# Kernel tuning notes

Hardware: AMD Instinct MI355X
Metric: run time of the kernel (lower is better)

## Reference

```python
import jax, jax.numpy as jnp
import numpy as np

N = 100000
E = 1600000
D = 128
L = 2
NEG_SLOPE = 0.2
LN_EPS = 1e-5


def setup_inputs() -> dict:
    key = jax.random.key(0)
    ks = jax.random.split(key, 12)
    x = jax.random.normal(ks[0], (N, D), dtype=jnp.float32)
    src = jax.random.randint(ks[1], (E,), 0, N)
    dst = jax.random.randint(ks[2], (E,), 0, N)
    dst = jnp.where(src == dst, (dst + 1) % N, dst)  # no pre-existing self-loops
    edge_index = jnp.stack([src, dst]).astype(jnp.int64)
    edge_weight = jax.random.uniform(ks[3], (E,), dtype=jnp.float32)
    s = 1.0 / np.sqrt(D)
    W = jax.random.normal(ks[4], (L, D, D), dtype=jnp.float32) * s
    att_src = jax.random.normal(ks[5], (L, D), dtype=jnp.float32) * s
    att_dst = jax.random.normal(ks[6], (L, D), dtype=jnp.float32) * s
    lin_edge_w = jax.random.normal(ks[7], (L, D), dtype=jnp.float32) * s  # Linear(1, D) weight
    att_edge = jax.random.normal(ks[8], (L, D), dtype=jnp.float32) * s
    bias = jnp.zeros((L, D), dtype=jnp.float32)
    ln_gamma = jnp.ones((D,), dtype=jnp.float32)
    ln_beta = jnp.zeros((D,), dtype=jnp.float32)
    return {"x": x, "edge_index": edge_index, "edge_weight": edge_weight,
            "W": W, "att_src": att_src, "att_dst": att_dst,
            "lin_edge_w": lin_edge_w, "att_edge": att_edge, "bias": bias,
            "ln_gamma": ln_gamma, "ln_beta": ln_beta}


def _gat_layer(x, src_f, dst_f, ew_f, W, a_src, a_dst, lew, a_edge, b):
    # x: [N, D]; src_f/dst_f/ew_f already include self-loops -> [E+N]
    h = x @ W                      # [N, D]
    alpha_s = h @ a_src            # [N]
    alpha_d = h @ a_dst            # [N]
    # edge_attr = ew[:,None] * lew; (edge_attr * att_edge).sum(-1) == ew * (lew . att_edge)
    alpha_e = ew_f * jnp.dot(lew, a_edge)           # [E+N]
    logits = jax.nn.leaky_relu(alpha_s[src_f] + alpha_d[dst_f] + alpha_e, NEG_SLOPE)
    # segment softmax over incoming edges of each destination node
    m = jax.ops.segment_max(logits, dst_f, num_segments=N)   # every node has a self-loop
    p = jnp.exp(logits - m[dst_f])
    z = jax.ops.segment_sum(p, dst_f, num_segments=N)
    coef = p / z[dst_f]                                      # [E+N]
    out = jax.ops.segment_sum(h[src_f] * coef[:, None], dst_f, num_segments=N)
    return out + b


def reference(x, edge_index, edge_weight, W, att_src, att_dst, lin_edge_w, att_edge, bias, ln_gamma, ln_beta):
    src, dst = edge_index[0], edge_index[1]
    # add_self_loops with fill_value='mean': loop weight = mean of incoming edge weights
    deg = jax.ops.segment_sum(jnp.ones_like(edge_weight), dst, num_segments=N)
    loop_w = jax.ops.segment_sum(edge_weight, dst, num_segments=N) / jnp.maximum(deg, 1.0)
    ar = jnp.arange(N)
    src_f = jnp.concatenate([src, ar])
    dst_f = jnp.concatenate([dst, ar])
    ew_f = jnp.concatenate([edge_weight, loop_w])
    xx = x
    for l in range(L):
        xx = _gat_layer(xx, src_f, dst_f, ew_f, W[l], att_src[l], att_dst[l],
                        lin_edge_w[l], att_edge[l], bias[l])
        xx = jax.nn.gelu(xx, approximate=False)
    xx = x + xx
    mu = jnp.mean(xx, axis=-1, keepdims=True)
    var = jnp.mean((xx - mu) ** 2, axis=-1, keepdims=True)
    return (xx - mu) * jax.lax.rsqrt(var + LN_EPS) * ln_gamma + ln_beta
```

## Files before the change

### kernel.cpp

```cpp
#include <hip/hip_runtime.h>
#include <hip/hip_bf16.h>
#include <math.h>

#define N_NODES 100000
#define N_EDGES 1600000
#define D 128
#define NEG 0.2f
#define LN_EPS 1e-5f

#define GEMM_BLOCKS ((N_NODES + 63) / 64)
#define PLACE_BLOCKS 1563

typedef __attribute__((ext_vector_type(8))) short bf16x8;
typedef __attribute__((ext_vector_type(4))) float f32x4;

__device__ __forceinline__ float lrelu(float v){ return fmaxf(v, NEG * v); }
__device__ __forceinline__ float gelu_exact(float v){ return 0.5f * v * (1.0f + erff(v * 0.7071067811865476f)); }
__device__ __forceinline__ float wave_sum(float v){
#pragma unroll
  for (int o = 32; o; o >>= 1) v += __shfl_xor(v, o, 64);
  return v;
}
__device__ __forceinline__ unsigned short f2bf(float f){
  __hip_bfloat16 h = __float2bfloat16(f);
  return *(unsigned short*)&h;
}
__device__ __forceinline__ float bf_lo(unsigned u){ return __uint_as_float(u << 16); }
__device__ __forceinline__ float bf_hi(unsigned u){ return __uint_as_float(u & 0xFFFF0000u); }

__global__ __launch_bounds__(256) void k_prep(const float* __restrict__ W,
                                              unsigned short* __restrict__ wfrag,
                                              const float* __restrict__ lew,
                                              const float* __restrict__ ae,
                                              float* __restrict__ c_e){
  if (threadIdx.x < 128){
    int l = threadIdx.x >> 6;
    int lane = threadIdx.x & 63;
    const float* a = lew + l * D;
    const float* b = ae + l * D;
    float v = a[lane] * b[lane] + a[64 + lane] * b[64 + lane];
    v = wave_sum(v);
    if (lane == 0) c_e[l] = v;
  }
#pragma unroll
  for (int it = 0; it < 16; it++){
    int slot = it * 256 + threadIdx.x;
    int lane = slot & 63;
    int kc   = (slot >> 6) & 3;
    int ct   = (slot >> 8) & 7;
    int l    = (slot >> 11) & 1;
    int quad = lane >> 4, n = (lane & 15) + ct * 16;
    const float* Wl = W + l * D * D;
    bf16x8 v;
#pragma unroll
    for (int j = 0; j < 8; j++){
      int k = kc * 32 + quad * 8 + j;
      v[j] = (short)f2bf(Wl[k * D + n]);
    }
    *(bf16x8*)(wfrag + (size_t)slot * 8) = v;
  }
}

__device__ __forceinline__ void gemm_mfma(int gb,
                                          const float* __restrict__ xin,
                                          const unsigned short* __restrict__ wfrag_l,
                                          const float* __restrict__ att_s,
                                          const float* __restrict__ att_d,
                                          unsigned short* __restrict__ hb,
                                          float* __restrict__ alpha_s,
                                          float* __restrict__ alpha_d){
  __shared__ __align__(16) unsigned short hstage[64 * 136];
  int tid = threadIdx.x;
  int wv = tid >> 6, lane = tid & 63;
  int quad = lane >> 4, c15 = lane & 15;
  int row0 = gb * 64 + wv * 16;

  int arow = min(row0 + c15, N_NODES - 1);
  const float* xr = xin + (size_t)arow * D;
  bf16x8 a[4];
#pragma unroll
  for (int kc = 0; kc < 4; kc++){
    float4 p = *(const float4*)(xr + kc * 32 + quad * 8);
    float4 q = *(const float4*)(xr + kc * 32 + quad * 8 + 4);
    bf16x8 t;
    t[0] = (short)f2bf(p.x); t[1] = (short)f2bf(p.y);
    t[2] = (short)f2bf(p.z); t[3] = (short)f2bf(p.w);
    t[4] = (short)f2bf(q.x); t[5] = (short)f2bf(q.y);
    t[6] = (short)f2bf(q.z); t[7] = (short)f2bf(q.w);
    a[kc] = t;
  }

  f32x4 acc[8];
#pragma unroll
  for (int ct = 0; ct < 8; ct++) acc[ct] = (f32x4){0.f, 0.f, 0.f, 0.f};

#pragma unroll
  for (int ct = 0; ct < 8; ct++){
#pragma unroll
    for (int kc = 0; kc < 4; kc++){
      bf16x8 b = *(const bf16x8*)(wfrag_l + ((size_t)(ct * 4 + kc) * 64 + lane) * 8);
      acc[ct] = __builtin_amdgcn_mfma_f32_16x16x32_bf16(a[kc], b, acc[ct], 0, 0, 0);
    }
  }

  float attsv[8], attdv[8];
#pragma unroll
  for (int ct = 0; ct < 8; ct++){
    attsv[ct] = att_s[ct * 16 + c15];
    attdv[ct] = att_d[ct * 16 + c15];
  }
#pragma unroll
  for (int reg = 0; reg < 4; reg++){
    float ps = 0.f, pd = 0.f;
#pragma unroll
    for (int ct = 0; ct < 8; ct++){
      ps += acc[ct][reg] * attsv[ct];
      pd += acc[ct][reg] * attdv[ct];
    }
#pragma unroll
    for (int o = 8; o; o >>= 1){
      ps += __shfl_xor(ps, o, 64);
      pd += __shfl_xor(pd, o, 64);
    }
    int row = row0 + quad * 4 + reg;
    if (c15 == reg && row < N_NODES){ alpha_s[row] = ps; alpha_d[row] = pd; }
  }

#pragma unroll
  for (int ct = 0; ct < 8; ct++)
#pragma unroll
    for (int reg = 0; reg < 4; reg++)
      hstage[(wv * 16 + quad * 4 + reg) * 136 + ct * 16 + c15] = f2bf(acc[ct][reg]);
  __syncthreads();
#pragma unroll
  for (int i = 0; i < 4; i++){
    int flat = i * 256 + tid;
    int row = flat >> 4, c = flat & 15;
    int grow = gb * 64 + row;
    if (grow < N_NODES)
      *(uint4*)(hb + (size_t)grow * D + c * 8) = *(const uint4*)(hstage + row * 136 + c * 8);
  }
}

__global__ __launch_bounds__(256, 4) void k_gemm1_place(const float* __restrict__ xin,
                                                        const unsigned short* __restrict__ wfrag,
                                                        const float* __restrict__ att_s,
                                                        const float* __restrict__ att_d,
                                                        unsigned short* __restrict__ hb,
                                                        float* __restrict__ alpha_s,
                                                        float* __restrict__ alpha_d,
                                                        const int* __restrict__ ei,
                                                        const float* __restrict__ ew,
                                                        int* __restrict__ counter,
                                                        int2* __restrict__ csr, int cap){
  if (blockIdx.x < GEMM_BLOCKS){
    gemm_mfma(blockIdx.x, xin, wfrag, att_s, att_d, hb, alpha_s, alpha_d);
  } else {
    int pb = blockIdx.x - GEMM_BLOCKS;
    int e0 = pb * 1024 + threadIdx.x;
    int ss[4], dd[4], pp[4]; float wwv[4]; bool va[4];
#pragma unroll
    for (int i = 0; i < 4; i++){
      int e = e0 + i * 256;
      va[i] = e < N_EDGES;
      ss[i] = va[i] ? ei[e] : 0;
      dd[i] = va[i] ? ei[N_EDGES + e] : 0;
      wwv[i] = va[i] ? ew[e] : 0.f;
    }
#pragma unroll
    for (int i = 0; i < 4; i++) if (va[i]) pp[i] = atomicAdd(&counter[dd[i]], 1);
#pragma unroll
    for (int i = 0; i < 4; i++)
      if (va[i] && pp[i] < cap)
        csr[(size_t)dd[i] * cap + pp[i]] = make_int2(ss[i], __float_as_int(wwv[i]));
  }
}

__global__ __launch_bounds__(256, 4) void k_gemm_alpha(const float* __restrict__ xin,
                                                       const unsigned short* __restrict__ wfrag,
                                                       const float* __restrict__ att_s,
                                                       const float* __restrict__ att_d,
                                                       unsigned short* __restrict__ hb,
                                                       float* __restrict__ alpha_s,
                                                       float* __restrict__ alpha_d){
  gemm_mfma(blockIdx.x, xin, wfrag, att_s, att_d, hb, alpha_s, alpha_d);
}

template<bool LN>
__global__ __launch_bounds__(256) void k_agg(const unsigned short* __restrict__ hb,
                                             const float* __restrict__ alpha_s,
                                             const float* __restrict__ alpha_d,
                                             const int* __restrict__ counter,
                                             const int2* __restrict__ csr, int cap,
                                             const float* __restrict__ c_e, int layer,
                                             const float* __restrict__ bias,
                                             const float* __restrict__ xres,
                                             const float* __restrict__ gamma,
                                             const float* __restrict__ beta,
                                             float* __restrict__ outp){
  int lane = threadIdx.x & 63;
  int cg = lane & 15;
  int qbase = lane & 48;
  int n = blockIdx.x * 16 + (threadIdx.x >> 4);
  float c = c_e[layer];
  int deg = counter[n];
  int dg = min(deg, cap);
  size_t rs = (size_t)n * cap;
  float ad = alpha_d[n];

  float z = 0.f, wsum = 0.f;
  float acc[8];
#pragma unroll
  for (int k = 0; k < 8; k++) acc[k] = 0.f;

  for (int base = 0; base < dg; base += 16){
    int j = base + cg;
    float p = 0.f; int s = 0;
    if (j < dg){
      int2 eg = csr[rs + j];
      s = eg.x;
      float w = __int_as_float(eg.y);
      wsum += w;
      p = __expf(lrelu(alpha_s[s] + ad + c * w));
    }
    z += p;
    int cnt = min(16, dg - base);
    for (int i = 0; i < cnt; i++){
      float pi = __shfl(p, qbase + i, 64);
      int   si = __shfl(s, qbase + i, 64);
      uint4 u = *((const uint4*)(hb + (size_t)si * D) + cg);
      acc[0] += pi * bf_lo(u.x); acc[1] += pi * bf_hi(u.x);
      acc[2] += pi * bf_lo(u.y); acc[3] += pi * bf_hi(u.y);
      acc[4] += pi * bf_lo(u.z); acc[5] += pi * bf_hi(u.z);
      acc[6] += pi * bf_lo(u.w); acc[7] += pi * bf_hi(u.w);
    }
  }
#pragma unroll
  for (int o = 8; o; o >>= 1){
    z += __shfl_xor(z, o, 64);
    wsum += __shfl_xor(wsum, o, 64);
  }

  float lw = wsum / fmaxf((float)deg, 1.0f);
  float ps = __expf(lrelu(alpha_s[n] + ad + c * lw));
  z += ps;
  uint4 u = *((const uint4*)(hb + (size_t)n * D) + cg);
  acc[0] += ps * bf_lo(u.x); acc[1] += ps * bf_hi(u.x);
  acc[2] += ps * bf_lo(u.y); acc[3] += ps * bf_hi(u.y);
  acc[4] += ps * bf_lo(u.z); acc[5] += ps * bf_hi(u.z);
  acc[6] += ps * bf_lo(u.w); acc[7] += ps * bf_hi(u.w);

  float inv = 1.0f / z;
  const float* b = bias + layer * D + cg * 8;
  float o[8];
#pragma unroll
  for (int k = 0; k < 8; k++) o[k] = gelu_exact(acc[k] * inv + b[k]);

  if constexpr (LN){
    const float* xr = xres + (size_t)n * D + cg * 8;
    float s1 = 0.f;
#pragma unroll
    for (int k = 0; k < 8; k++){ o[k] += xr[k]; s1 += o[k]; }
#pragma unroll
    for (int ofs = 8; ofs; ofs >>= 1) s1 += __shfl_xor(s1, ofs, 64);
    float mu = s1 * (1.0f / D);
    float s2 = 0.f;
#pragma unroll
    for (int k = 0; k < 8; k++){ o[k] -= mu; s2 += o[k] * o[k]; }
#pragma unroll
    for (int ofs = 8; ofs; ofs >>= 1) s2 += __shfl_xor(s2, ofs, 64);
    float rinv = rsqrtf(s2 * (1.0f / D) + LN_EPS);
    const float* g = gamma + cg * 8;
    const float* bt = beta + cg * 8;
#pragma unroll
    for (int k = 0; k < 8; k++) o[k] = o[k] * rinv * g[k] + bt[k];
  }

  float* orow = outp + (size_t)n * D + cg * 8;
  *(float4*)(orow)     = make_float4(o[0], o[1], o[2], o[3]);
  *(float4*)(orow + 4) = make_float4(o[4], o[5], o[6], o[7]);
}

extern "C" void kernel_launch(void* const* d_in, const int* in_sizes, int n_in,
                              void* d_out, int out_size, void* d_ws, size_t ws_size,
                              hipStream_t stream) {
  const float* x     = (const float*)d_in[0];
  const int*   ei    = (const int*)d_in[1];
  const float* ew    = (const float*)d_in[2];
  const float* W     = (const float*)d_in[3];
  const float* att_s = (const float*)d_in[4];
  const float* att_d = (const float*)d_in[5];
  const float* lew   = (const float*)d_in[6];
  const float* ae    = (const float*)d_in[7];
  const float* bias  = (const float*)d_in[8];
  const float* gamma = (const float*)d_in[9];
  const float* beta  = (const float*)d_in[10];
  float* out = (float*)d_out;

  const int N = N_NODES;

  size_t fixed = (size_t)(3 * N + 16) * 4 + 65536;
  size_t need64 = fixed + (size_t)N * 64 * 8 + (size_t)N * D * 2;
  int cap = (ws_size >= need64) ? 64 : 48;

  int*   counter  = (int*)d_ws;
  float* alpha_s  = (float*)(counter + N);
  float* alpha_d  = alpha_s + N;
  float* c_e      = alpha_d + N;
  unsigned short* wfrag = (unsigned short*)(c_e + 16);
  int2*  csr      = (int2*)(wfrag + 32768);
  unsigned short* hb = (unsigned short*)(csr + (size_t)N * cap);

  hipMemsetAsync(counter, 0, (size_t)N * sizeof(int), stream);
  k_prep<<<1, 256, 0, stream>>>(W, wfrag, lew, ae, c_e);

  k_gemm1_place<<<GEMM_BLOCKS + PLACE_BLOCKS, 256, 0, stream>>>(
      x, wfrag, att_s, att_d, hb, alpha_s, alpha_d, ei, ew, counter, csr, cap);

  k_agg<false><<<N / 16, 256, 0, stream>>>(hb, alpha_s, alpha_d, counter, csr, cap,
                                           c_e, 0, bias, nullptr, nullptr, nullptr, out);

  k_gemm_alpha<<<GEMM_BLOCKS, 256, 0, stream>>>(out, wfrag + 16384, att_s + D, att_d + D,
                                                hb, alpha_s, alpha_d);
  k_agg<true><<<N / 16, 256, 0, stream>>>(hb, alpha_s, alpha_d, counter, csr, cap,
                                          c_e, 1, bias, x, gamma, beta, out);
}
```

Before: 487.6 us.

## Fuse layer-1 aggregation with layer-2 GEMM and pack edges into 32 bits

The layer-1 aggregation now feeds its GELU output straight through shared memory into the layer-2 MFMA GEMM and alpha projections. This removes the fp32 intermediate write, its re-read, and one kernel launch. CSR entries are packed into a single 32-bit word holding a 17-bit source index and a 15-bit quantized edge weight, halving CSR traffic. The counter memset moves into the prep kernel and the place loop handles 8 edges per thread. The quantized weight adds approximation error, and the packing only holds while node ids fit in 17 bits.

```diff
diff --git a/kernel.cpp b/kernel.cpp
--- a/kernel.cpp
+++ b/kernel.cpp
@@ -9,7 +9,8 @@
 #define LN_EPS 1e-5f
 
 #define GEMM_BLOCKS ((N_NODES + 63) / 64)
-#define PLACE_BLOCKS 1563
+#define EPT 8
+#define PLACE_BLOCKS ((N_EDGES + 256*EPT - 1) / (256*EPT))
 
 typedef __attribute__((ext_vector_type(8))) short bf16x8;
 typedef __attribute__((ext_vector_type(4))) float f32x4;
@@ -27,24 +28,22 @@
 }
 __device__ __forceinline__ float bf_lo(unsigned u){ return __uint_as_float(u << 16); }
 __device__ __forceinline__ float bf_hi(unsigned u){ return __uint_as_float(u & 0xFFFF0000u); }
+
+__device__ __forceinline__ unsigned pack_edge(int s, float w){
+  int q = (int)(w * 32768.0f + 0.5f);
+  q = min(q, 32767);
+  return ((unsigned)s << 15) | (unsigned)q;
+}
 
 __global__ __launch_bounds__(256) void k_prep(const float* __restrict__ W,
                                               unsigned short* __restrict__ wfrag,
                                               const float* __restrict__ lew,
                                               const float* __restrict__ ae,
-                                              float* __restrict__ c_e){
-  if (threadIdx.x < 128){
-    int l = threadIdx.x >> 6;
-    int lane = threadIdx.x & 63;
-    const float* a = lew + l * D;
-    const float* b = ae + l * D;
-    float v = a[lane] * b[lane] + a[64 + lane] * b[64 + lane];
-    v = wave_sum(v);
-    if (lane == 0) c_e[l] = v;
-  }
-#pragma unroll
-  for (int it = 0; it < 16; it++){
-    int slot = it * 256 + threadIdx.x;
+                                              float* __restrict__ c_e,
+                                              int* __restrict__ counter){
+  int b = blockIdx.x;
+  if (b < 16){
+    int slot = b * 256 + threadIdx.x;
     int lane = slot & 63;
     int kc   = (slot >> 6) & 3;
     int ct   = (slot >> 8) & 7;
@@ -58,6 +57,19 @@
       v[j] = (short)f2bf(Wl[k * D + n]);
     }
     *(bf16x8*)(wfrag + (size_t)slot * 8) = v;
+  } else if (b == 16){
+    if (threadIdx.x < 128){
+      int l = threadIdx.x >> 6;
+      int lane = threadIdx.x & 63;
+      const float* a = lew + l * D;
+      const float* bb = ae + l * D;
+      float v = a[lane] * bb[lane] + a[64 + lane] * bb[64 + lane];
+      v = wave_sum(v);
+      if (lane == 0) c_e[l] = v;
+    }
+  } else {
+    int i = (b - 17) * 256 + threadIdx.x;
+    if (i < N_NODES) counter[i] = 0;
   }
 }
 
@@ -93,15 +105,13 @@
   f32x4 acc[8];
 #pragma unroll
   for (int ct = 0; ct < 8; ct++) acc[ct] = (f32x4){0.f, 0.f, 0.f, 0.f};
-
-#pragma unroll
-  for (int ct = 0; ct < 8; ct++){
+#pragma unroll
+  for (int ct = 0; ct < 8; ct++)
 #pragma unroll
     for (int kc = 0; kc < 4; kc++){
       bf16x8 b = *(const bf16x8*)(wfrag_l + ((size_t)(ct * 4 + kc) * 64 + lane) * 8);
       acc[ct] = __builtin_amdgcn_mfma_f32_16x16x32_bf16(a[kc], b, acc[ct], 0, 0, 0);
     }
-  }
 
   float attsv[8], attdv[8];
 #pragma unroll
@@ -152,57 +162,39 @@
                                                         const int* __restrict__ ei,
                                                         const float* __restrict__ ew,
                                                         int* __restrict__ counter,
-                                                        int2* __restrict__ csr, int cap){
+                                                        unsigned* __restrict__ csr, int cap){
   if (blockIdx.x < GEMM_BLOCKS){
     gemm_mfma(blockIdx.x, xin, wfrag, att_s, att_d, hb, alpha_s, alpha_d);
   } else {
     int pb = blockIdx.x - GEMM_BLOCKS;
-    int e0 = pb * 1024 + threadIdx.x;
-    int ss[4], dd[4], pp[4]; float wwv[4]; bool va[4];
-#pragma unroll
-    for (int i = 0; i < 4; i++){
+    int e0 = pb * (256 * EPT) + threadIdx.x;
+    int dd[EPT], pp[EPT]; unsigned pk[EPT]; bool va[EPT];
+#pragma unroll
+    for (int i = 0; i < EPT; i++){
       int e = e0 + i * 256;
       va[i] = e < N_EDGES;
-      ss[i] = va[i] ? ei[e] : 0;
+      int s = va[i] ? ei[e] : 0;
       dd[i] = va[i] ? ei[N_EDGES + e] : 0;
-      wwv[i] = va[i] ? ew[e] : 0.f;
-    }
-#pragma unroll
-    for (int i = 0; i < 4; i++) if (va[i]) pp[i] = atomicAdd(&counter[dd[i]], 1);
-#pragma unroll
-    for (int i = 0; i < 4; i++)
-      if (va[i] && pp[i] < cap)
-        csr[(size_t)dd[i] * cap + pp[i]] = make_int2(ss[i], __float_as_int(wwv[i]));
-  }
-}
-
-__global__ __launch_bounds__(256, 4) void k_gemm_alpha(const float* __restrict__ xin,
-                                                       const unsigned short* __restrict__ wfrag,
-                                                       const float* __restrict__ att_s,
-                                                       const float* __restrict__ att_d,
-                                                       unsigned short* __restrict__ hb,
-                                                       float* __restrict__ alpha_s,
-                                                       float* __restrict__ alpha_d){
-  gemm_mfma(blockIdx.x, xin, wfrag, att_s, att_d, hb, alpha_s, alpha_d);
-}
-
-template<bool LN>
-__global__ __launch_bounds__(256) void k_agg(const unsigned short* __restrict__ hb,
-                                             const float* __restrict__ alpha_s,
-                                             const float* __restrict__ alpha_d,
-                                             const int* __restrict__ counter,
-                                             const int2* __restrict__ csr, int cap,
-                                             const float* __restrict__ c_e, int layer,
-                                             const float* __restrict__ bias,
-                                             const float* __restrict__ xres,
-                                             const float* __restrict__ gamma,
-                                             const float* __restrict__ beta,
-                                             float* __restrict__ outp){
-  int lane = threadIdx.x & 63;
+      float w = va[i] ? ew[e] : 0.f;
+      pk[i] = pack_edge(s, w);
+    }
+#pragma unroll
+    for (int i = 0; i < EPT; i++) if (va[i]) pp[i] = atomicAdd(&counter[dd[i]], 1);
+#pragma unroll
+    for (int i = 0; i < EPT; i++)
+      if (va[i] && pp[i] < cap) csr[(size_t)dd[i] * cap + pp[i]] = pk[i];
+  }
+}
+
+__device__ __forceinline__ void agg_node(const unsigned short* __restrict__ hb,
+                                         const float* __restrict__ alpha_s,
+                                         const float* __restrict__ alpha_d,
+                                         const int* __restrict__ counter,
+                                         const unsigned* __restrict__ csr, int cap,
+                                         float c, const float* __restrict__ bias_l,
+                                         int n, int lane, float o[8]){
   int cg = lane & 15;
   int qbase = lane & 48;
-  int n = blockIdx.x * 16 + (threadIdx.x >> 4);
-  float c = c_e[layer];
   int deg = counter[n];
   int dg = min(deg, cap);
   size_t rs = (size_t)n * cap;
@@ -217,9 +209,9 @@
     int j = base + cg;
     float p = 0.f; int s = 0;
     if (j < dg){
-      int2 eg = csr[rs + j];
-      s = eg.x;
-      float w = __int_as_float(eg.y);
+      unsigned u = csr[rs + j];
+      s = (int)(u >> 15);
+      float w = (float)(u & 32767u) * (1.0f / 32768.0f);
       wsum += w;
       p = __expf(lrelu(alpha_s[s] + ad + c * w));
     }
@@ -228,53 +220,160 @@
     for (int i = 0; i < cnt; i++){
       float pi = __shfl(p, qbase + i, 64);
       int   si = __shfl(s, qbase + i, 64);
-      uint4 u = *((const uint4*)(hb + (size_t)si * D) + cg);
-      acc[0] += pi * bf_lo(u.x); acc[1] += pi * bf_hi(u.x);
-      acc[2] += pi * bf_lo(u.y); acc[3] += pi * bf_hi(u.y);
-      acc[4] += pi * bf_lo(u.z); acc[5] += pi * bf_hi(u.z);
-      acc[6] += pi * bf_lo(u.w); acc[7] += pi * bf_hi(u.w);
-    }
-  }
-#pragma unroll
-  for (int o = 8; o; o >>= 1){
-    z += __shfl_xor(z, o, 64);
-    wsum += __shfl_xor(wsum, o, 64);
+      uint4 u4 = *((const uint4*)(hb + (size_t)si * D) + cg);
+      acc[0] += pi * bf_lo(u4.x); acc[1] += pi * bf_hi(u4.x);
+      acc[2] += pi * bf_lo(u4.y); acc[3] += pi * bf_hi(u4.y);
+      acc[4] += pi * bf_lo(u4.z); acc[5] += pi * bf_hi(u4.z);
+      acc[6] += pi * bf_lo(u4.w); acc[7] += pi * bf_hi(u4.w);
+    }
+  }
+#pragma unroll
+  for (int o2 = 8; o2; o2 >>= 1){
+    z += __shfl_xor(z, o2, 64);
+    wsum += __shfl_xor(wsum, o2, 64);
   }
 
   float lw = wsum / fmaxf((float)deg, 1.0f);
   float ps = __expf(lrelu(alpha_s[n] + ad + c * lw));
   z += ps;
-  uint4 u = *((const uint4*)(hb + (size_t)n * D) + cg);
-  acc[0] += ps * bf_lo(u.x); acc[1] += ps * bf_hi(u.x);
-  acc[2] += ps * bf_lo(u.y); acc[3] += ps * bf_hi(u.y);
-  acc[4] += ps * bf_lo(u.z); acc[5] += ps * bf_hi(u.z);
-  acc[6] += ps * bf_lo(u.w); acc[7] += ps * bf_hi(u.w);
+  uint4 u4 = *((const uint4*)(hb + (size_t)n * D) + cg);
+  acc[0] += ps * bf_lo(u4.x); acc[1] += ps * bf_hi(u4.x);
+  acc[2] += ps * bf_lo(u4.y); acc[3] += ps * bf_hi(u4.y);
+  acc[4] += ps * bf_lo(u4.z); acc[5] += ps * bf_hi(u4.z);
+  acc[6] += ps * bf_lo(u4.w); acc[7] += ps * bf_hi(u4.w);
 
   float inv = 1.0f / z;
-  const float* b = bias + layer * D + cg * 8;
+  const float* b = bias_l + cg * 8;
+#pragma unroll
+  for (int k = 0; k < 8; k++) o[k] = gelu_exact(acc[k] * inv + b[k]);
+}
+
+__global__ __launch_bounds__(256, 4) void k_agg_gemm(const unsigned short* __restrict__ h1,
+                                                     const float* __restrict__ as1,
+                                                     const float* __restrict__ ad1,
+                                                     const int* __restrict__ counter,
+                                                     const unsigned* __restrict__ csr, int cap,
+                                                     const float* __restrict__ c_e,
+                                                     const float* __restrict__ bias,
+                                                     const unsigned short* __restrict__ wfrag2,
+                                                     const float* __restrict__ att_s2,
+                                                     const float* __restrict__ att_d2,
+                                                     unsigned short* __restrict__ h2,
+                                                     float* __restrict__ as2,
+                                                     float* __restrict__ ad2){
+  __shared__ __align__(16) float Xs[16 * 132];
+  __shared__ __align__(16) unsigned short hstage[16 * 136];
+  __shared__ float aps[4][16], apd[4][16];
+  int tid = threadIdx.x, lane = tid & 63, wv = tid >> 6;
+  int quad = lane >> 4, c15 = lane & 15;
+  int rnode = tid >> 4;
+  int row0 = blockIdx.x * 16;
+  int n = row0 + rnode;
+
   float o[8];
-#pragma unroll
-  for (int k = 0; k < 8; k++) o[k] = gelu_exact(acc[k] * inv + b[k]);
-
-  if constexpr (LN){
-    const float* xr = xres + (size_t)n * D + cg * 8;
-    float s1 = 0.f;
-#pragma unroll
-    for (int k = 0; k < 8; k++){ o[k] += xr[k]; s1 += o[k]; }
-#pragma unroll
-    for (int ofs = 8; ofs; ofs >>= 1) s1 += __shfl_xor(s1, ofs, 64);
-    float mu = s1 * (1.0f / D);
-    float s2 = 0.f;
-#pragma unroll
-    for (int k = 0; k < 8; k++){ o[k] -= mu; s2 += o[k] * o[k]; }
-#pragma unroll
-    for (int ofs = 8; ofs; ofs >>= 1) s2 += __shfl_xor(s2, ofs, 64);
-    float rinv = rsqrtf(s2 * (1.0f / D) + LN_EPS);
-    const float* g = gamma + cg * 8;
-    const float* bt = beta + cg * 8;
-#pragma unroll
-    for (int k = 0; k < 8; k++) o[k] = o[k] * rinv * g[k] + bt[k];
-  }
+  agg_node(h1, as1, ad1, counter, csr, cap, c_e[0], bias, n, lane, o);
+
+  int cg = lane & 15;
+  float* xr = Xs + rnode * 132 + cg * 8;
+  *(float4*)(xr)     = make_float4(o[0], o[1], o[2], o[3]);
+  *(float4*)(xr + 4) = make_float4(o[4], o[5], o[6], o[7]);
+  __syncthreads();
+
+  bf16x8 a[4];
+#pragma unroll
+  for (int kc = 0; kc < 4; kc++){
+    const float* src = Xs + c15 * 132 + kc * 32 + quad * 8;
+    float4 p = *(const float4*)(src);
+    float4 q = *(const float4*)(src + 4);
+    bf16x8 t;
+    t[0] = (short)f2bf(p.x); t[1] = (short)f2bf(p.y);
+    t[2] = (short)f2bf(p.z); t[3] = (short)f2bf(p.w);
+    t[4] = (short)f2bf(q.x); t[5] = (short)f2bf(q.y);
+    t[6] = (short)f2bf(q.z); t[7] = (short)f2bf(q.w);
+    a[kc] = t;
+  }
+
+  f32x4 acc2[2];
+#pragma unroll
+  for (int t = 0; t < 2; t++) acc2[t] = (f32x4){0.f, 0.f, 0.f, 0.f};
+#pragma unroll
+  for (int t = 0; t < 2; t++){
+    int ct = wv * 2 + t;
+#pragma unroll
+    for (int kc = 0; kc < 4; kc++){
+      bf16x8 b = *(const bf16x8*)(wfrag2 + ((size_t)(ct * 4 + kc) * 64 + lane) * 8);
+      acc2[t] = __builtin_amdgcn_mfma_f32_16x16x32_bf16(a[kc], b, acc2[t], 0, 0, 0);
+    }
+  }
+
+  float attsv[2], attdv[2];
+#pragma unroll
+  for (int t = 0; t < 2; t++){
+    attsv[t] = att_s2[(wv * 2 + t) * 16 + c15];
+    attdv[t] = att_d2[(wv * 2 + t) * 16 + c15];
+  }
+#pragma unroll
+  for (int reg = 0; reg < 4; reg++){
+    float ps = acc2[0][reg] * attsv[0] + acc2[1][reg] * attsv[1];
+    float pd = acc2[0][reg] * attdv[0] + acc2[1][reg] * attdv[1];
+#pragma unroll
+    for (int of = 8; of; of >>= 1){
+      ps += __shfl_xor(ps, of, 64);
+      pd += __shfl_xor(pd, of, 64);
+    }
+    if (c15 == reg){ aps[wv][quad * 4 + reg] = ps; apd[wv][quad * 4 + reg] = pd; }
+  }
+#pragma unroll
+  for (int t = 0; t < 2; t++)
+#pragma unroll
+    for (int reg = 0; reg < 4; reg++)
+      hstage[(quad * 4 + reg) * 136 + (wv * 2 + t) * 16 + c15] = f2bf(acc2[t][reg]);
+  __syncthreads();
+
+  if (tid < 16){
+    as2[row0 + tid] = aps[0][tid] + aps[1][tid] + aps[2][tid] + aps[3][tid];
+    ad2[row0 + tid] = apd[0][tid] + apd[1][tid] + apd[2][tid] + apd[3][tid];
+  }
+  {
+    int row = tid >> 4, c = tid & 15;
+    *(uint4*)(h2 + (size_t)(row0 + row) * D + c * 8) = *(const uint4*)(hstage + row * 136 + c * 8);
+  }
+}
+
+__global__ __launch_bounds__(256) void k_agg2(const unsigned short* __restrict__ h2,
+                                              const float* __restrict__ as2,
+                                              const float* __restrict__ ad2,
+                                              const int* __restrict__ counter,
+                                              const unsigned* __restrict__ csr, int cap,
+                                              const float* __restrict__ c_e,
+                                              const float* __restrict__ bias,
+                                              const float* __restrict__ xres,
+                                              const float* __restrict__ gamma,
+                                              const float* __restrict__ beta,
+                                              float* __restrict__ outp){
+  int lane = threadIdx.x & 63;
+  int cg = lane & 15;
+  int n = blockIdx.x * 16 + (threadIdx.x >> 4);
+  float o[8];
+  agg_node(h2, as2, ad2, counter, csr, cap, c_e[1], bias + D, n, lane, o);
+
+  const float* xr = xres + (size_t)n * D + cg * 8;
+  float s1 = 0.f;
+#pragma unroll
+  for (int k = 0; k < 8; k++){ o[k] += xr[k]; s1 += o[k]; }
+#pragma unroll
+  for (int of = 8; of; of >>= 1) s1 += __shfl_xor(s1, of, 64);
+  float mu = s1 * (1.0f / D);
+  float s2 = 0.f;
+#pragma unroll
+  for (int k = 0; k < 8; k++){ o[k] -= mu; s2 += o[k] * o[k]; }
+#pragma unroll
+  for (int of = 8; of; of >>= 1) s2 += __shfl_xor(s2, of, 64);
+  float rinv = rsqrtf(s2 * (1.0f / D) + LN_EPS);
+  const float* g = gamma + cg * 8;
+  const float* bt = beta + cg * 8;
+#pragma unroll
+  for (int k = 0; k < 8; k++) o[k] = o[k] * rinv * g[k] + bt[k];
 
   float* orow = outp + (size_t)n * D + cg * 8;
   *(float4*)(orow)     = make_float4(o[0], o[1], o[2], o[3]);
@@ -299,29 +398,35 @@
 
   const int N = N_NODES;
 
-  size_t fixed = (size_t)(3 * N + 16) * 4 + 65536;
-  size_t need64 = fixed + (size_t)N * 64 * 8 + (size_t)N * D * 2;
-  int cap = (ws_size >= need64) ? 64 : 48;
-
-  int*   counter  = (int*)d_ws;
-  float* alpha_s  = (float*)(counter + N);
-  float* alpha_d  = alpha_s + N;
-  float* c_e      = alpha_d + N;
+  size_t fixed = (size_t)(5 * N + 16) * 4 + 65536 + (size_t)N * D * 2 * 2;
+  int cap = 64;
+  if (ws_size < fixed + (size_t)N * 64 * 4){
+    size_t avail = (ws_size > fixed) ? (ws_size - fixed) : 0;
+    cap = (int)(avail / ((size_t)N * 4));
+    if (cap > 64) cap = 64;
+    if (cap < 44) cap = 44;
+  }
+
+  int*   counter = (int*)d_ws;
+  float* as1     = (float*)(counter + N);
+  float* ad1     = as1 + N;
+  float* as2     = ad1 + N;
+  float* ad2     = as2 + N;
+  float* c_e     = ad2 + N;
   unsigned short* wfrag = (unsigned short*)(c_e + 16);
-  int2*  csr      = (int2*)(wfrag + 32768);
-  unsigned short* hb = (unsigned short*)(csr + (size_t)N * cap);
-
-  hipMemsetAsync(counter, 0, (size_t)N * sizeof(int), stream);
-  k_prep<<<1, 256, 0, stream>>>(W, wfrag, lew, ae, c_e);
+  unsigned* csr  = (unsigned*)(wfrag + 32768);
+  unsigned short* h1 = (unsigned short*)(csr + (size_t)N * cap);
+  unsigned short* h2 = h1 + (size_t)N * D;
+
+  k_prep<<<17 + (N + 255) / 256, 256, 0, stream>>>(W, wfrag, lew, ae, c_e, counter);
 
   k_gemm1_place<<<GEMM_BLOCKS + PLACE_BLOCKS, 256, 0, stream>>>(
-      x, wfrag, att_s, att_d, hb, alpha_s, alpha_d, ei, ew, counter, csr, cap);
-
-  k_agg<false><<<N / 16, 256, 0, stream>>>(hb, alpha_s, alpha_d, counter, csr, cap,
-                                           c_e, 0, bias, nullptr, nullptr, nullptr, out);
-
-  k_gemm_alpha<<<GEMM_BLOCKS, 256, 0, stream>>>(out, wfrag + 16384, att_s + D, att_d + D,
-                                                hb, alpha_s, alpha_d);
-  k_agg<true><<<N / 16, 256, 0, stream>>>(hb, alpha_s, alpha_d, counter, csr, cap,
-                                          c_e, 1, bias, x, gamma, beta, out);
-}
+      x, wfrag, att_s, att_d, h1, as1, ad1, ei, ew, counter, csr, cap);
+
+  k_agg_gemm<<<N / 16, 256, 0, stream>>>(h1, as1, ad1, counter, csr, cap, c_e, bias,
+                                         wfrag + 16384, att_s + D, att_d + D,
+                                         h2, as2, ad2);
+
+  k_agg2<<<N / 16, 256, 0, stream>>>(h2, as2, ad2, counter, csr, cap, c_e, bias,
+                                     x, gamma, beta, out);
+}
```

After: 490.5 us. About the same (+0.6%).
